# Kernel tuning notes

Measured on AMD Instinct MI355X. Metric: run time of the kernel, lower is better.

The kernel has to match this reference:

```python
import jax, jax.numpy as jnp
import numpy as np

N_HEADS = 16
EMBED_DIM = 1024
HEAD_DIM = EMBED_DIM // N_HEADS
SEQ_LEN = 2048


def setup_inputs() -> dict:
    key = jax.random.key(0)
    ks = jax.random.split(key, 9)
    s = 1.0 / np.sqrt(EMBED_DIM)
    inp = {
        "x": jax.random.normal(ks[0], (SEQ_LEN, EMBED_DIM), dtype=jnp.float32),
        "Wq": jax.random.uniform(ks[1], (EMBED_DIM, EMBED_DIM), jnp.float32, -s, s),
        "bq": jax.random.uniform(ks[2], (EMBED_DIM,), jnp.float32, -s, s),
        "Wk": jax.random.uniform(ks[3], (EMBED_DIM, EMBED_DIM), jnp.float32, -s, s),
        "bk": jax.random.uniform(ks[4], (EMBED_DIM,), jnp.float32, -s, s),
        "Wv": jax.random.uniform(ks[5], (EMBED_DIM, EMBED_DIM), jnp.float32, -s, s),
        "bv": jax.random.uniform(ks[6], (EMBED_DIM,), jnp.float32, -s, s),
        "Wo": jax.random.uniform(ks[7], (EMBED_DIM, EMBED_DIM), jnp.float32, -s, s),
        "bo": jax.random.uniform(ks[8], (EMBED_DIM,), jnp.float32, -s, s),
    }
    return inp


def reference(x, Wq, bq, Wk, bk, Wv, bv, Wo, bo):
    # Linear layers (torch convention: y = x @ W.T + b)
    Q = x @ Wq.T + bq  # [S, E]
    K = x @ Wk.T + bk
    V = x @ Wv.T + bv
    # split heads -> [H, S, D]
    def split(t):
        return t.reshape(SEQ_LEN, N_HEADS, HEAD_DIM).transpose(1, 0, 2)
    Qh, Kh, Vh = split(Q), split(K), split(V)
    # NOTE: faithful to source, scale is sqrt(embed_dim), not sqrt(head_dim)
    scale = 1.0 / np.sqrt(EMBED_DIM)
    scores = jnp.einsum("hsd,htd->hst", Qh, Kh) * scale  # [H, S, S]
    attn = jax.nn.softmax(scores, axis=-1)
    ctx = jnp.einsum("hst,htd->hsd", attn, Vh)  # [H, S, D]
    ctx = ctx.transpose(1, 0, 2).reshape(SEQ_LEN, EMBED_DIM)
    out = ctx @ Wo.T + bo
    return (out, attn)
```

## Files before the change

### kernel.cpp

```cpp
#include <hip/hip_runtime.h>
#include <hip/hip_bf16.h>
#include <stdint.h>

#define SQL 2048
#define EMB 1024
#define NHD 16
#define HDD 64

typedef __bf16 bf16x8 __attribute__((ext_vector_type(8)));
typedef __bf16 bf16x4 __attribute__((ext_vector_type(4)));
typedef float f32x4 __attribute__((ext_vector_type(4)));
typedef float f32x16 __attribute__((ext_vector_type(16)));

__device__ __forceinline__ f32x4 mfma16(bf16x8 a, bf16x8 b, f32x4 c) {
    return __builtin_amdgcn_mfma_f32_16x16x32_bf16(a, b, c, 0, 0, 0);
}
__device__ __forceinline__ f32x16 mfma32(bf16x8 a, bf16x8 b, f32x16 c) {
    return __builtin_amdgcn_mfma_f32_32x32x16_bf16(a, b, c, 0, 0, 0);
}

__device__ __forceinline__ void gload_lds16(const __bf16* g, __bf16* lds) {
    __builtin_amdgcn_global_load_lds(
        (const __attribute__((address_space(1))) uint32_t*)g,
        (__attribute__((address_space(3))) uint32_t*)lds,
        16, 0, 0);
}

__global__ void cast5_kernel(const float* __restrict__ x, const float* __restrict__ wq,
                             const float* __restrict__ wk, const float* __restrict__ wv,
                             const float* __restrict__ wo, __bf16* __restrict__ out)
{
    int i = blockIdx.x * blockDim.x + threadIdx.x;
    const float* src; int off;
    if      (i < (512 << 10))  { src = x;  off = 0; }
    else if (i < (768 << 10))  { src = wq; off = 512 << 10; }
    else if (i < (1024 << 10)) { src = wk; off = 768 << 10; }
    else if (i < (1280 << 10)) { src = wv; off = 1024 << 10; }
    else                       { src = wo; off = 1280 << 10; }
    float4 v = ((const float4*)src)[i - off];
    bf16x4 o;
    o[0] = (__bf16)v.x; o[1] = (__bf16)v.y; o[2] = (__bf16)v.z; o[3] = (__bf16)v.w;
    ((bf16x4*)out)[i] = o;
}

template<bool OUT_BF16, bool TRZ2>
__global__ __launch_bounds__(256, 2)
void gemm_bt(const __bf16* __restrict__ A,
             const __bf16* __restrict__ B0, const __bf16* __restrict__ B1, const __bf16* __restrict__ B2,
             const float* __restrict__ bias0, const float* __restrict__ bias1, const float* __restrict__ bias2,
             void* __restrict__ out0, void* __restrict__ out1, void* __restrict__ out2,
             float s0, float s1, float s2,
             int M, int N, int K)
{
    const __bf16* B = B0; const float* bias = bias0; void* Cout = out0; float cscale = s0;
    if (blockIdx.z == 1) { B = B1; bias = bias1; Cout = out1; cscale = s1; }
    if (blockIdx.z == 2) { B = B2; bias = bias2; Cout = out2; cscale = s2; }

    __shared__ __attribute__((aligned(16))) __bf16 As[128 * 32];
    __shared__ __attribute__((aligned(16))) __bf16 Bs[128 * 32];

    const int tid  = threadIdx.x;
    const int lane = tid & 63;
    const int wave = tid >> 6;
    const int lrow = lane & 15;
    const int quad = lane >> 4;
    const int bm = blockIdx.y * 128;
    const int bn = blockIdx.x * 128;
    const int wm = (wave >> 1) * 64;
    const int wn = (wave & 1) * 64;

    const f32x4 fzero = {0.f, 0.f, 0.f, 0.f};
    f32x4 acc[4][4];
#pragma unroll
    for (int i = 0; i < 4; i++)
#pragma unroll
        for (int j = 0; j < 4; j++) acc[i][j] = fzero;

    const int srow = (lane >> 2);
    const int scol = (lane & 3) * 8;

    for (int k0 = 0; k0 < K; k0 += 32) {
        __syncthreads();
#pragma unroll
        for (int i = 0; i < 2; i++) {
            int rbase = wave * 32 + i * 16;
            gload_lds16(&A[(size_t)(bm + rbase + srow) * K + k0 + scol], &As[rbase * 32]);
            gload_lds16(&B[(size_t)(bn + rbase + srow) * K + k0 + scol], &Bs[rbase * 32]);
        }
        __syncthreads();
        bf16x8 af[4], bfr[4];
#pragma unroll
        for (int i = 0; i < 4; i++) af[i]  = *(const bf16x8*)&As[(wm + i * 16 + lrow) * 32 + quad * 8];
#pragma unroll
        for (int i = 0; i < 4; i++) bfr[i] = *(const bf16x8*)&Bs[(wn + i * 16 + lrow) * 32 + quad * 8];
#pragma unroll
        for (int mi = 0; mi < 4; mi++)
#pragma unroll
            for (int ni = 0; ni < 4; ni++)
                acc[mi][ni] = mfma16(af[mi], bfr[ni], acc[mi][ni]);
    }

    const bool trz = TRZ2 && (blockIdx.z == 2);
#pragma unroll
    for (int mi = 0; mi < 4; mi++) {
        int row = bm + wm + mi * 16 + quad * 4;
#pragma unroll
        for (int ni = 0; ni < 4; ni++) {
            int col = bn + wn + ni * 16 + lrow;
            float bv = bias[col];
            if (trz) {
                bf16x4 t;
#pragma unroll
                for (int r = 0; r < 4; r++) t[r] = (__bf16)((acc[mi][ni][r] + bv) * cscale);
                *(bf16x4*)&((__bf16*)Cout)[(size_t)col * SQL + row] = t;
            } else {
#pragma unroll
                for (int r = 0; r < 4; r++) {
                    float v = (acc[mi][ni][r] + bv) * cscale;
                    if (OUT_BF16) ((__bf16*)Cout)[(size_t)(row + r) * N + col] = (__bf16)v;
                    else          ((float*)Cout)[(size_t)(row + r) * N + col] = v;
                }
            }
        }
    }
}

__global__ __launch_bounds__(256, 2)
void attn_kernel(const __bf16* __restrict__ Qg, const __bf16* __restrict__ Kg,
                 const __bf16* __restrict__ Vt, float* __restrict__ attn,
                 __bf16* __restrict__ ctx)
{
    __shared__ __attribute__((aligned(16))) __bf16 Ks[2][64 * 64];
    __shared__ __attribute__((aligned(16))) __bf16 Vs[2][64 * 64];
    __shared__ __attribute__((aligned(16))) float  Pf[2][64 * 68];
    __shared__ float Lb[4][64];
    float* Ored = &Pf[0][0];

    const int tid  = threadIdx.x;
    const int lane = tid & 63;
    const int w    = tid >> 6;
    const int wq   = w & 1;
    const int wk   = w >> 1;
    const int l31  = lane & 31;
    const int hi   = lane >> 5;

    const int b    = blockIdx.x;
    const int xcd  = b & 7;
    const int slot = b >> 3;
    const int h    = xcd + ((slot >> 5) << 3);
    const int q0   = (slot & 31) * 64;

    const f32x16 Z16 = {0.f,0.f,0.f,0.f,0.f,0.f,0.f,0.f,0.f,0.f,0.f,0.f,0.f,0.f,0.f,0.f};

    bf16x8 qf[2][4];
#pragma unroll
    for (int qg = 0; qg < 2; qg++) {
        const __bf16* qp = &Qg[(size_t)(q0 + qg * 32 + l31) * EMB + h * HDD + hi * 8];
#pragma unroll
        for (int ds = 0; ds < 4; ds++) qf[qg][ds] = *(const bf16x8*)&qp[ds * 16];
    }

    {
        const __bf16* kp = &Kg[(size_t)(w * 32 + l31) * EMB + h * HDD + hi * 8];
        const size_t tstep = (size_t)128 * EMB;
        bf16x8 kcur[4], knxt[4];
#pragma unroll
        for (int ds = 0; ds < 4; ds++) kcur[ds] = *(const bf16x8*)&kp[ds * 16];
        float ls0 = 0.f, ls1 = 0.f;
        for (int t = 0; t < 16; t++) {
            if (t < 15) {
#pragma unroll
                for (int ds = 0; ds < 4; ds++)
                    knxt[ds] = *(const bf16x8*)&kp[(size_t)(t + 1) * tstep + ds * 16];
            }
            f32x16 sA = Z16, sB = Z16;
#pragma unroll
            for (int ds = 0; ds < 4; ds++) {
                sA = mfma32(kcur[ds], qf[0][ds], sA);
                sB = mfma32(kcur[ds], qf[1][ds], sB);
            }
#pragma unroll
            for (int r = 0; r < 16; r++) { ls0 += __expf(sA[r]); ls1 += __expf(sB[r]); }
            if (t < 15) {
#pragma unroll
                for (int ds = 0; ds < 4; ds++) kcur[ds] = knxt[ds];
            }
        }
        ls0 += __shfl_xor(ls0, 32);
        ls1 += __shfl_xor(ls1, 32);
        if (hi == 0) { Lb[w][l31] = ls0; Lb[w][32 + l31] = ls1; }
    }

    const int srow  = lane >> 3;
    const int sslot = (lane & 7) ^ (srow & 7);
    auto stageK = [&](int buf, int k0) {
#pragma unroll
        for (int j = 0; j < 2; j++) {
            int r = w * 16 + j * 8;
            gload_lds16(&Kg[(size_t)(k0 + r + srow) * EMB + h * HDD + sslot * 8],
                        &Ks[buf][r * 64]);
        }
    };
    auto stageV = [&](int buf, int k0) {
#pragma unroll
        for (int j = 0; j < 2; j++) {
            int r = w * 16 + j * 8;
            gload_lds16(&Vt[(size_t)(h * HDD + r + srow) * SQL + k0 + sslot * 8],
                        &Vs[buf][r * 64]);
        }
    };

    stageK(0, 0);
    stageV(0, 0);
    __syncthreads();

    float rinv;
    {
        int q = wq * 32 + l31;
        rinv = 1.f / (Lb[0][q] + Lb[1][q] + Lb[2][q] + Lb[3][q]);
    }

    f32x16 o0 = Z16, o1 = Z16;
    float* __restrict__ attn_h = attn + (size_t)h * SQL * SQL;
    const int krowoff = (wk * 32 + l31) * 64;
    const int lane7   = lane & 7;
    const int vrow0 = l31 * 64;
    const int vrow1 = (32 + l31) * 64;
    const int pq    = (wq * 32 + l31) * 68;
    const bf16x8* qfp = qf[wq];

    int buf = 0;
    for (int t = 0; t < 32; t++) {
        const int k0 = t * 64;
        if (t < 31) { stageK(buf ^ 1, k0 + 64); stageV(buf ^ 1, k0 + 64); }
        f32x16 s = Z16;
#pragma unroll
        for (int ds = 0; ds < 4; ds++) {
            bf16x8 kf = *(const bf16x8*)&Ks[buf][krowoff + ((((ds << 1) | hi) ^ lane7) << 3)];
            s = mfma32(kf, qfp[ds], s);
        }
#pragma unroll
        for (int g = 0; g < 4; g++) {
            f32x4 pv;
#pragma unroll
            for (int i = 0; i < 4; i++) pv[i] = __expf(s[g * 4 + i]) * rinv;
            *(f32x4*)&Pf[buf][pq + wk * 32 + g * 8 + hi * 4] = pv;
        }
#pragma unroll
        for (int kt = 0; kt < 2; kt++) {
            const float* pp = &Pf[buf][pq + wk * 32 + kt * 16 + hi * 8];
            f32x4 pA = *(const f32x4*)pp;
            f32x4 pB = *(const f32x4*)(pp + 4);
            bf16x8 pf;
#pragma unroll
            for (int i = 0; i < 4; i++) { pf[i] = (__bf16)pA[i]; pf[i + 4] = (__bf16)pB[i]; }
            int vslot = (((wk << 2) | (kt << 1) | hi) ^ lane7) << 3;
            bf16x8 v0 = *(const bf16x8*)&Vs[buf][vrow0 + vslot];
            bf16x8 v1 = *(const bf16x8*)&Vs[buf][vrow1 + vslot];
            o0 = mfma32(v0, pf, o0);
            o1 = mfma32(v1, pf, o1);
        }
        __syncthreads();
#pragma unroll
        for (int j = 0; j < 4; j++) {
            int lin = j * 256 + tid;
            int r   = lin >> 4;
            int c   = (lin & 15) << 2;
            f32x4 v = *(const f32x4*)&Pf[buf][r * 68 + c];
            __builtin_nontemporal_store(v, (f32x4*)&attn_h[(size_t)(q0 + r) * SQL + k0 + c]);
        }
        buf ^= 1;
    }

    if (wk == 1) {
#pragma unroll
        for (int g = 0; g < 4; g++)
#pragma unroll
            for (int i = 0; i < 4; i++) {
                int dl = i + g * 8 + hi * 4;
                Ored[dl * 66 + wq * 32 + l31]        = o0[g * 4 + i];
                Ored[(32 + dl) * 66 + wq * 32 + l31] = o1[g * 4 + i];
            }
    }
    __syncthreads();
    if (wk == 0) {
        __bf16* crow = &ctx[(size_t)(q0 + wq * 32 + l31) * EMB + h * HDD];
#pragma unroll
        for (int g = 0; g < 4; g++) {
            bf16x4 c0, c1;
#pragma unroll
            for (int i = 0; i < 4; i++) {
                int dl = i + g * 8 + hi * 4;
                c0[i] = (__bf16)(o0[g * 4 + i] + Ored[dl * 66 + wq * 32 + l31]);
                c1[i] = (__bf16)(o1[g * 4 + i] + Ored[(32 + dl) * 66 + wq * 32 + l31]);
            }
            *(bf16x4*)&crow[g * 8 + hi * 4]      = c0;
            *(bf16x4*)&crow[32 + g * 8 + hi * 4] = c1;
        }
    }
}

extern "C" void kernel_launch(void* const* d_in, const int* in_sizes, int n_in,
                              void* d_out, int out_size, void* d_ws, size_t ws_size,
                              hipStream_t stream)
{
    const float* x  = (const float*)d_in[0];
    const float* Wq = (const float*)d_in[1];
    const float* bq = (const float*)d_in[2];
    const float* Wk = (const float*)d_in[3];
    const float* bk = (const float*)d_in[4];
    const float* Wv = (const float*)d_in[5];
    const float* bv = (const float*)d_in[6];
    const float* Wo = (const float*)d_in[7];
    const float* bo = (const float*)d_in[8];

    float* out  = (float*)d_out;
    float* attn = out + (size_t)SQL * EMB;

    const size_t M1 = 1u << 20;
    __bf16* wsb = (__bf16*)d_ws;
    __bf16* xb  = wsb;
    __bf16* wqb = wsb + 2 * M1;
    __bf16* wkb = wsb + 3 * M1;
    __bf16* wvb = wsb + 4 * M1;
    __bf16* wob = wsb + 5 * M1;
    __bf16* Qb  = wsb + 6 * M1;
    __bf16* Kb  = wsb + 8 * M1;
    __bf16* Vtb = wsb + 12 * M1;
    __bf16* ctb = wsb + 14 * M1;

    cast5_kernel<<<6144, 256, 0, stream>>>(x, Wq, Wk, Wv, Wo, wsb);

    gemm_bt<true, true><<<dim3(EMB / 128, SQL / 128, 3), 256, 0, stream>>>(
        xb, wqb, wkb, wvb, bq, bk, bv,
        (void*)Qb, (void*)Kb, (void*)Vtb,
        0.03125f, 1.0f, 1.0f, SQL, EMB, EMB);

    attn_kernel<<<512, 256, 0, stream>>>(Qb, Kb, Vtb, attn, ctb);

    gemm_bt<false, false><<<dim3(EMB / 128, SQL / 128, 1), 256, 0, stream>>>(
        ctb, wob, wob, wob, bo, bo, bo,
        (void*)out, (void*)out, (void*)out,
        1.0f, 1.0f, 1.0f, SQL, EMB, EMB);
}
```

Baseline: 396.3 us.

## Double-buffer GEMM LDS tiles with swizzle and XCD-aware block mapping

Rewrites the projection GEMM main loop to stage 64-wide K tiles into two LDS buffers, prefetching the next tile while MFMAs run on the current one, with a single barrier per step. LDS rows are XOR-swizzled to avoid bank conflicts on fragment reads. A 1D grid remaps blocks so each XCD handles a fixed weight column tile, improving L2 reuse. LDS use doubles (64KB per block), which may reduce occupancy.

```diff
diff --git a/kernel.cpp b/kernel.cpp
--- a/kernel.cpp
+++ b/kernel.cpp
@@ -50,22 +50,30 @@
              const float* __restrict__ bias0, const float* __restrict__ bias1, const float* __restrict__ bias2,
              void* __restrict__ out0, void* __restrict__ out1, void* __restrict__ out2,
              float s0, float s1, float s2,
-             int M, int N, int K)
+             int M, int N, int K, int nmtiles)
 {
+    const int b    = blockIdx.x;
+    const int xcd  = b & 7;
+    const int idx  = b >> 3;
+    const int p    = idx / nmtiles;
+    const int bm_i = idx - p * nmtiles;
+    const int pid  = xcd + 8 * p;
+    const int bn   = (pid & 7) * 128;
+    const int bm   = bm_i * 128;
+    const int z    = pid >> 3;
+
     const __bf16* B = B0; const float* bias = bias0; void* Cout = out0; float cscale = s0;
-    if (blockIdx.z == 1) { B = B1; bias = bias1; Cout = out1; cscale = s1; }
-    if (blockIdx.z == 2) { B = B2; bias = bias2; Cout = out2; cscale = s2; }
-
-    __shared__ __attribute__((aligned(16))) __bf16 As[128 * 32];
-    __shared__ __attribute__((aligned(16))) __bf16 Bs[128 * 32];
+    if (z == 1) { B = B1; bias = bias1; Cout = out1; cscale = s1; }
+    if (z == 2) { B = B2; bias = bias2; Cout = out2; cscale = s2; }
+
+    __shared__ __attribute__((aligned(16))) __bf16 As[2][128 * 64];
+    __shared__ __attribute__((aligned(16))) __bf16 Bs[2][128 * 64];
 
     const int tid  = threadIdx.x;
     const int lane = tid & 63;
     const int wave = tid >> 6;
     const int lrow = lane & 15;
     const int quad = lane >> 4;
-    const int bm = blockIdx.y * 128;
-    const int bn = blockIdx.x * 128;
     const int wm = (wave >> 1) * 64;
     const int wn = (wave & 1) * 64;
 
@@ -76,31 +84,50 @@
 #pragma unroll
         for (int j = 0; j < 4; j++) acc[i][j] = fzero;
 
-    const int srow = (lane >> 2);
-    const int scol = (lane & 3) * 8;
-
-    for (int k0 = 0; k0 < K; k0 += 32) {
+    const int srow  = lane >> 3;
+    const int sslot = (lane & 7) ^ srow;
+
+    auto stage = [&](int sbuf, int k0) {
+#pragma unroll
+        for (int j = 0; j < 4; j++) {
+            int r0 = wave * 32 + j * 8;
+            gload_lds16(&A[(size_t)(bm + r0 + srow) * K + k0 + sslot * 8], &As[sbuf][r0 * 64]);
+            gload_lds16(&B[(size_t)(bn + r0 + srow) * K + k0 + sslot * 8], &Bs[sbuf][r0 * 64]);
+        }
+    };
+
+    const int nt = K >> 6;
+    int buf = 0;
+    stage(0, 0);
+    __syncthreads();
+
+    for (int t = 0; t < nt; t++) {
+        if (t < nt - 1) stage(buf ^ 1, (t + 1) * 64);
+        bf16x8 af[4][2], bfr[4][2];
+#pragma unroll
+        for (int i = 0; i < 4; i++) {
+            int ra = wm + i * 16 + lrow;
+            int rb = wn + i * 16 + lrow;
+#pragma unroll
+            for (int ks = 0; ks < 2; ks++) {
+                int sa = (((ks << 2) | quad) ^ (ra & 7)) << 3;
+                int sb = (((ks << 2) | quad) ^ (rb & 7)) << 3;
+                af[i][ks]  = *(const bf16x8*)&As[buf][ra * 64 + sa];
+                bfr[i][ks] = *(const bf16x8*)&Bs[buf][rb * 64 + sb];
+            }
+        }
+#pragma unroll
+        for (int ks = 0; ks < 2; ks++)
+#pragma unroll
+            for (int mi = 0; mi < 4; mi++)
+#pragma unroll
+                for (int ni = 0; ni < 4; ni++)
+                    acc[mi][ni] = mfma16(af[mi][ks], bfr[ni][ks], acc[mi][ni]);
         __syncthreads();
-#pragma unroll
-        for (int i = 0; i < 2; i++) {
-            int rbase = wave * 32 + i * 16;
-            gload_lds16(&A[(size_t)(bm + rbase + srow) * K + k0 + scol], &As[rbase * 32]);
-            gload_lds16(&B[(size_t)(bn + rbase + srow) * K + k0 + scol], &Bs[rbase * 32]);
-        }
-        __syncthreads();
-        bf16x8 af[4], bfr[4];
-#pragma unroll
-        for (int i = 0; i < 4; i++) af[i]  = *(const bf16x8*)&As[(wm + i * 16 + lrow) * 32 + quad * 8];
-#pragma unroll
-        for (int i = 0; i < 4; i++) bfr[i] = *(const bf16x8*)&Bs[(wn + i * 16 + lrow) * 32 + quad * 8];
-#pragma unroll
-        for (int mi = 0; mi < 4; mi++)
-#pragma unroll
-            for (int ni = 0; ni < 4; ni++)
-                acc[mi][ni] = mfma16(af[mi], bfr[ni], acc[mi][ni]);
-    }
-
-    const bool trz = TRZ2 && (blockIdx.z == 2);
+        buf ^= 1;
+    }
+
+    const bool trz = TRZ2 && (z == 2);
 #pragma unroll
     for (int mi = 0; mi < 4; mi++) {
         int row = bm + wm + mi * 16 + quad * 4;
@@ -331,15 +358,15 @@
 
     cast5_kernel<<<6144, 256, 0, stream>>>(x, Wq, Wk, Wv, Wo, wsb);
 
-    gemm_bt<true, true><<<dim3(EMB / 128, SQL / 128, 3), 256, 0, stream>>>(
+    gemm_bt<true, true><<<384, 256, 0, stream>>>(
         xb, wqb, wkb, wvb, bq, bk, bv,
         (void*)Qb, (void*)Kb, (void*)Vtb,
-        0.03125f, 1.0f, 1.0f, SQL, EMB, EMB);
+        0.03125f, 1.0f, 1.0f, SQL, EMB, EMB, 16);
 
     attn_kernel<<<512, 256, 0, stream>>>(Qb, Kb, Vtb, attn, ctb);
 
-    gemm_bt<false, false><<<dim3(EMB / 128, SQL / 128, 1), 256, 0, stream>>>(
+    gemm_bt<false, false><<<128, 256, 0, stream>>>(
         ctb, wob, wob, wob, bo, bo, bo,
         (void*)out, (void*)out, (void*)out,
-        1.0f, 1.0f, 1.0f, SQL, EMB, EMB);
-}
+        1.0f, 1.0f, 1.0f, SQL, EMB, EMB, 16);
+}
```

After: 388.5 us. About the same (-2.0%).
